# Kernel tuning notes

Hardware: AMD Instinct MI355X
Metric: run time of the kernel (lower is better)

## Reference

```python
import jax, jax.numpy as jnp
import numpy as np

COV_EMB = 32
N_HEAD = 2
FACTOR_TCL = 2   # TemporalConvolutionalLayer factor (default 2)
FACTOR_MLP = 1   # MLP factor passed from MultiAttention init
EPS = 1e-5


def _conv1d_causal(x, w, b):
    # x: [N, C, T], w: [O, C, 3]; torch pads 2 both sides then slices [..., :-2],
    # equivalent to left-pad 2 only -> output length T.
    y = jax.lax.conv_general_dilated(x, w, window_strides=(1,), padding=[(2, 0)],
                                     dimension_numbers=('NCH', 'OIH', 'NCH'))
    return y + b[None, :, None]


def _tcl(x, w_conv, b_conv, w_proj, b_proj):
    # TemporalConvolutionalLayer: x [..., T, C] -> [..., T, C]
    shp = x.shape
    T, C = shp[-2], shp[-1]
    x2 = x.reshape(-1, T, C).transpose(0, 2, 1)              # [N, C, T]
    h = jax.nn.gelu(_conv1d_causal(x2, w_conv, b_conv), approximate=False)
    h = h.transpose(0, 2, 1)                                  # [N, T, 2C]
    out = h @ w_proj.T + b_proj                               # [N, T, C]
    return out.reshape(*shp[:-1], C)


def _layernorm(x, w):
    mu = jnp.mean(x, axis=-1, keepdims=True)
    var = jnp.var(x, axis=-1, keepdims=True)
    return (x - mu) * jax.lax.rsqrt(var + EPS) * w


def setup_inputs() -> dict:
    key = jax.random.key(0)
    ks = jax.random.split(key, 20)
    C = COV_EMB
    C2 = FACTOR_TCL * C
    s = 0.02
    inp = {
        'causal_decoder': jax.random.normal(ks[0], (8, 4, 1024, C), jnp.float32),
        'past_kv': jax.random.normal(ks[1], (8, 1024, C), jnp.float32),
    }
    def tcl_params(i):
        return (jax.random.normal(ks[i], (C2, C, 3), jnp.float32) * s,
                jnp.zeros((C2,), jnp.float32),
                jax.random.normal(ks[i + 1], (C, C2), jnp.float32) * s,
                jnp.zeros((C,), jnp.float32))
    inp['wq_conv'], inp['bq_conv'], inp['wq_proj'], inp['bq_proj'] = tcl_params(2)
    inp['wk_conv'], inp['bk_conv'], inp['wk_proj'], inp['bk_proj'] = tcl_params(4)
    inp['wv_conv'], inp['bv_conv'], inp['wv_proj'], inp['bv_proj'] = tcl_params(6)
    inp['w_cproj'] = jax.random.normal(ks[8], (C, C), jnp.float32) * s   # bias=False
    inp['ln_w'] = jnp.ones((C,), jnp.float32)                            # bias=False
    inp['w_fc'] = jax.random.normal(ks[9], (FACTOR_MLP * C, C), jnp.float32) * s   # bias=False
    inp['w_mlp_proj'] = jax.random.normal(ks[10], (C, FACTOR_MLP * C), jnp.float32) * s
    return inp


def reference(causal_decoder, past_kv,
              wq_conv, bq_conv, wq_proj, bq_proj,
              wk_conv, bk_conv, wk_proj, bk_proj,
              wv_conv, bv_conv, wv_proj, bv_proj,
              w_cproj, ln_w, w_fc, w_mlp_proj):
    B, F, T, C = causal_decoder.shape
    nh, hd = N_HEAD, C // N_HEAD

    q = _tcl(causal_decoder, wq_conv, bq_conv, wq_proj, bq_proj)   # [B,F,T,C]
    k = _tcl(past_kv, wk_conv, bk_conv, wk_proj, bk_proj)          # [B,S,C]
    v = _tcl(past_kv, wv_conv, bv_conv, wv_proj, bv_proj)          # [B,S,C]

    S = k.shape[1]
    q = q.reshape(B, F, T, nh, hd).transpose(0, 1, 3, 2, 4)        # [B,F,h,T,d]
    k = k.reshape(B, S, nh, hd).transpose(0, 2, 1, 3)              # [B,h,S,d]
    v = v.reshape(B, S, nh, hd).transpose(0, 2, 1, 3)              # [B,h,S,d]

    scale = 1.0 / jnp.sqrt(jnp.asarray(hd, q.dtype))
    scores = jnp.einsum('bfhtd,bhsd->bfhts', q, k) * scale          # [B,F,h,T,S]
    attn = jax.nn.softmax(scores, axis=-1)
    y = jnp.einsum('bfhts,bhsd->bfhtd', attn, v)                    # [B,F,h,T,d]
    y = y.transpose(0, 1, 3, 2, 4).reshape(B, F, T, C)

    out = causal_decoder + y @ w_cproj.T                            # resid_dropout = id (p=0)
    h = _layernorm(out, ln_w)
    mlp = jax.nn.gelu(h @ w_fc.T, approximate=False) @ w_mlp_proj.T
    out = out + mlp
    return out
```

## Files before the change

kernel.cpp:

```cpp
#include <hip/hip_runtime.h>
#include <hip/hip_bf16.h>

#define T_LEN 1024

typedef __attribute__((ext_vector_type(8))) short short8;
typedef __attribute__((ext_vector_type(4))) short short4v;
typedef __attribute__((ext_vector_type(4))) float float4v;
typedef __attribute__((ext_vector_type(2))) unsigned uint2v;
typedef __attribute__((ext_vector_type(4))) unsigned uint4v;

__device__ __forceinline__ float gelu_exact(float x) {
    return 0.5f * x * (1.0f + erff(x * 0.70710678118654752440f));
}
__device__ __forceinline__ unsigned short f2bf(float f) {
    unsigned u = __float_as_uint(f);
    u += 0x7fffu + ((u >> 16) & 1u);
    return (unsigned short)(u >> 16);
}
__device__ __forceinline__ unsigned pk2bf(float a, float b) {
    __hip_bfloat162 h = __float22bfloat162_rn(make_float2(a, b));
    unsigned u;
    __builtin_memcpy(&u, &h, 4);
    return u;
}
__device__ __forceinline__ float fexp2(float x) {
    float r;
    asm("v_exp_f32 %0, %1" : "=v"(r) : "v"(x));
    return r;
}

__device__ __forceinline__ short8 xpose_p(float4v t0, float4v t1) {
    unsigned u0 = pk2bf(t0.x, t0.y);
    unsigned u1 = pk2bf(t0.z, t0.w);
    unsigned u2 = pk2bf(t1.x, t1.y);
    unsigned u3 = pk2bf(t1.z, t1.w);
    uint2v r0 = __builtin_amdgcn_permlane32_swap(u0, u2, false, false);
    uint2v r1 = __builtin_amdgcn_permlane32_swap(u1, u3, false, false);
    uint2v r2 = __builtin_amdgcn_permlane16_swap(r0.x, r0.y, false, false);
    uint2v r3 = __builtin_amdgcn_permlane16_swap(r1.x, r1.y, false, false);
    uint4v p = { r2.x, r3.x, r2.y, r3.y };
    short8 f;
    __builtin_memcpy(&f, &p, 16);
    return f;
}

__global__ __launch_bounds__(256) void kv_tcl(
    const float* __restrict__ pkv,
    const float* __restrict__ wkc, const float* __restrict__ bkc,
    const float* __restrict__ wkp, const float* __restrict__ bkp,
    const float* __restrict__ wvc, const float* __restrict__ bvc,
    const float* __restrict__ wvp, const float* __restrict__ bvp,
    unsigned short* __restrict__ kbf, unsigned short* __restrict__ vtbf)
{
    __shared__ __align__(16) unsigned short Abuf[32 * 96];
    __shared__ __align__(16) unsigned short WbT[64 * 96];
    __shared__ __align__(16) unsigned short Hb[32 * 72];
    __shared__ __align__(16) unsigned short WpB[32 * 72];

    const int tid = threadIdx.x;
    const int gb = blockIdx.x;

    const float *wc, *bc, *wp, *bp;
    unsigned short* outb;
    int n, mode;
    if (gb < 256) { n = gb >> 5;         wc = wkc; bc = bkc; wp = wkp; bp = bkp; outb = kbf;  mode = 0; }
    else          { n = (gb - 256) >> 5; wc = wvc; bc = bvc; wp = wvp; bp = bvp; outb = vtbf; mode = 1; }
    const int t0 = (gb & 31) * 32;

#pragma unroll
    for (int it = 0; it < 3; ++it) {
        int s = (tid + it * 256) >> 3;
        int sub = tid & 7;
        int t = s / 3, tap = s - t * 3;
        int tau = t0 + t - 2 + tap;
        float4 xv = make_float4(0.f, 0.f, 0.f, 0.f);
        if (tau >= 0) xv = *(const float4*)&pkv[((size_t)n * T_LEN + tau) * 32 + sub * 4];
        short4v pk = { (short)f2bf(xv.x), (short)f2bf(xv.y),
                       (short)f2bf(xv.z), (short)f2bf(xv.w) };
        *(short4v*)&Abuf[t * 96 + tap * 32 + sub * 4] = pk;
    }
#pragma unroll
    for (int it = 0; it < 6; ++it) {
        int i4 = tid + it * 256;
        int idx = i4 * 4;
        int o = idx / 96, r = idx - o * 96;
        float4 w4 = *(const float4*)&wc[idx];
        float we[4] = { w4.x, w4.y, w4.z, w4.w };
#pragma unroll
        for (int e = 0; e < 4; ++e) {
            int re = r + e, c = re / 3, tap = re - c * 3;
            WbT[o * 96 + tap * 32 + c] = f2bf(we[e]);
        }
    }
#pragma unroll
    for (int it = 0; it < 2; ++it) {
        int i4 = tid + it * 256;
        int idx = i4 * 4;
        int c = idx >> 6, o = idx & 63;
        float4 w4 = *(const float4*)&wp[idx];
        short4v pk = { (short)f2bf(w4.x), (short)f2bf(w4.y),
                       (short)f2bf(w4.z), (short)f2bf(w4.w) };
        *(short4v*)&WpB[c * 72 + o] = pk;
    }

    const int w = tid >> 6;
    const int ln = tid & 63;
    const int sn = ln & 15;
    const int quad = ln >> 4;

    const float bcv = bc[w * 16 + sn];
    const int tmw = w & 1, cnw = w >> 1;
    const float bpv = bp[cnw * 16 + sn];

    __syncthreads();

    short8 b0 = *(const short8*)&WbT[(w * 16 + sn) * 96 + 0  + quad * 8];
    short8 b1 = *(const short8*)&WbT[(w * 16 + sn) * 96 + 32 + quad * 8];
    short8 b2 = *(const short8*)&WbT[(w * 16 + sn) * 96 + 64 + quad * 8];
    float4v zero = { 0.f, 0.f, 0.f, 0.f };
    float4v acc[2] = { zero, zero };
#pragma unroll
    for (int tm = 0; tm < 2; ++tm) {
        const unsigned short* ar = &Abuf[(tm * 16 + sn) * 96 + quad * 8];
        short8 a0 = *(const short8*)(ar + 0);
        short8 a1 = *(const short8*)(ar + 32);
        short8 a2 = *(const short8*)(ar + 64);
        acc[tm] = __builtin_amdgcn_mfma_f32_16x16x32_bf16(a0, b0, acc[tm], 0, 0, 0);
        acc[tm] = __builtin_amdgcn_mfma_f32_16x16x32_bf16(a1, b1, acc[tm], 0, 0, 0);
        acc[tm] = __builtin_amdgcn_mfma_f32_16x16x32_bf16(a2, b2, acc[tm], 0, 0, 0);
    }
#pragma unroll
    for (int tm = 0; tm < 2; ++tm) {
        float ge[4];
        ge[0] = gelu_exact(acc[tm].x + bcv);
        ge[1] = gelu_exact(acc[tm].y + bcv);
        ge[2] = gelu_exact(acc[tm].z + bcv);
        ge[3] = gelu_exact(acc[tm].w + bcv);
#pragma unroll
        for (int i = 0; i < 4; ++i)
            Hb[(tm * 16 + quad * 4 + i) * 72 + w * 16 + sn] = f2bf(ge[i]);
    }

    __syncthreads();

    const unsigned short* hr = &Hb[(tmw * 16 + sn) * 72 + quad * 8];
    short8 pa0 = *(const short8*)(hr + 0);
    short8 pa1 = *(const short8*)(hr + 32);
    short8 pb0 = *(const short8*)&WpB[(cnw * 16 + sn) * 72 + quad * 8];
    short8 pb1 = *(const short8*)&WpB[(cnw * 16 + sn) * 72 + 32 + quad * 8];
    float4v pacc = zero;
    pacc = __builtin_amdgcn_mfma_f32_16x16x32_bf16(pa0, pb0, pacc, 0, 0, 0);
    pacc = __builtin_amdgcn_mfma_f32_16x16x32_bf16(pa1, pb1, pacc, 0, 0, 0);

    float v[4] = { pacc.x + bpv, pacc.y + bpv, pacc.z + bpv, pacc.w + bpv };
#pragma unroll
    for (int i = 0; i < 4; ++i) {
        int t = tmw * 16 + quad * 4 + i;
        int c = cnw * 16 + sn;
        if (mode == 0) {
            outb[((size_t)n * T_LEN + t0 + t) * 32 + c] = f2bf(v[i]);
        } else {
            outb[((size_t)(n * 2 + cnw) * 16 + sn) * T_LEN + t0 + t] = f2bf(v[i]);
        }
    }
}

__global__ __launch_bounds__(1024, 8) void fused_qae(
    const float* __restrict__ cd,
    const float* __restrict__ wqc, const float* __restrict__ bqc,
    const float* __restrict__ wqp, const float* __restrict__ bqp,
    const unsigned short* __restrict__ kbf,
    const unsigned short* __restrict__ vtbf,
    const float* __restrict__ wcp, const float* __restrict__ lnw,
    const float* __restrict__ wfc, const float* __restrict__ wmp,
    float* __restrict__ out)
{
    __shared__ __align__(16) char smem[52736];
    unsigned short* Abuf = (unsigned short*)(smem);
    unsigned short* WbT  = (unsigned short*)(smem + 12288);
    unsigned short* Hb   = (unsigned short*)(smem + 24576);
    unsigned short* WpB  = (unsigned short*)(smem + 33792);
    unsigned short* qs   = (unsigned short*)(smem + 38400);

    const int tid = threadIdx.x;
    const int bf = blockIdx.x >> 4;
    const int tt = blockIdx.x & 15;
    const int t0 = tt * 64;
    const int b = bf >> 2;
    const float SC = 0.36067376022224085f;

#pragma unroll
    for (int it = 0; it < 2; ++it) {
        int idx = tid + it * 1024;
        if (idx < 1536) {
            int s = idx >> 3;
            int sub = idx & 7;
            int t = s / 3, tap = s - t * 3;
            int tau = t0 + t - 2 + tap;
            float4 xv = make_float4(0.f, 0.f, 0.f, 0.f);
            if (tau >= 0) xv = *(const float4*)&cd[((size_t)bf * T_LEN + tau) * 32 + sub * 4];
            short4v pk = { (short)f2bf(xv.x), (short)f2bf(xv.y),
                           (short)f2bf(xv.z), (short)f2bf(xv.w) };
            *(short4v*)&Abuf[t * 96 + tap * 32 + sub * 4] = pk;
        }
    }
#pragma unroll
    for (int it = 0; it < 2; ++it) {
        int i4 = tid + it * 1024;
        if (i4 < 1536) {
            int idx = i4 * 4;
            int o = idx / 96, r = idx - o * 96;
            float4 w4 = *(const float4*)&wqc[idx];
            float we[4] = { w4.x, w4.y, w4.z, w4.w };
#pragma unroll
            for (int e = 0; e < 4; ++e) {
                int re = r + e, c = re / 3, tap = re - c * 3;
                WbT[o * 96 + tap * 32 + c] = f2bf(we[e]);
            }
        }
    }
    if (tid < 512) {
        int idx = tid * 4;
        int c = idx >> 6, o = idx & 63;
        float4 w4 = *(const float4*)&wqp[idx];
        short4v pk = { (short)f2bf(w4.x), (short)f2bf(w4.y),
                       (short)f2bf(w4.z), (short)f2bf(w4.w) };
        *(short4v*)&WpB[c * 72 + o] = pk;
    }

    const int w = tid >> 6;
    const int ln = tid & 63;
    const int sn = ln & 15;
    const int quad = ln >> 4;
    const float4v zero = { 0.f, 0.f, 0.f, 0.f };

    __syncthreads();

    {
        const int tm = w & 3;
        const int on = w >> 2;
        const unsigned short* ar = &Abuf[(tm * 16 + sn) * 96 + quad * 8];
        short8 a0 = *(const short8*)(ar + 0);
        short8 a1 = *(const short8*)(ar + 32);
        short8 a2 = *(const short8*)(ar + 64);
        const unsigned short* br = &WbT[(on * 16 + sn) * 96 + quad * 8];
        float4v c0 = zero;
        c0 = __builtin_amdgcn_mfma_f32_16x16x32_bf16(a0, *(const short8*)(br + 0),  c0, 0, 0, 0);
        c0 = __builtin_amdgcn_mfma_f32_16x16x32_bf16(a1, *(const short8*)(br + 32), c0, 0, 0, 0);
        c0 = __builtin_amdgcn_mfma_f32_16x16x32_bf16(a2, *(const short8*)(br + 64), c0, 0, 0, 0);
        const float bc0 = bqc[on * 16 + sn];
        float g0[4] = { gelu_exact(c0.x + bc0), gelu_exact(c0.y + bc0),
                        gelu_exact(c0.z + bc0), gelu_exact(c0.w + bc0) };
#pragma unroll
        for (int i = 0; i < 4; ++i)
            Hb[(tm * 16 + quad * 4 + i) * 72 + on * 16 + sn] = f2bf(g0[i]);
    }
    __syncthreads();

    if (w < 8) {
        const int tm = w & 3, cn = w >> 2;
        const unsigned short* hr = &Hb[(tm * 16 + sn) * 72 + quad * 8];
        short8 pa0 = *(const short8*)(hr + 0);
        short8 pa1 = *(const short8*)(hr + 32);
        const unsigned short* wr_ = &WpB[(cn * 16 + sn) * 72 + quad * 8];
        short8 pb0 = *(const short8*)(wr_ + 0);
        short8 pb1 = *(const short8*)(wr_ + 32);
        float4v pacc = zero;
        pacc = __builtin_amdgcn_mfma_f32_16x16x32_bf16(pa0, pb0, pacc, 0, 0, 0);
        pacc = __builtin_amdgcn_mfma_f32_16x16x32_bf16(pa1, pb1, pacc, 0, 0, 0);
        const float bpv = bqp[cn * 16 + sn];
        float v[4] = { (pacc.x + bpv) * SC, (pacc.y + bpv) * SC,
                       (pacc.z + bpv) * SC, (pacc.w + bpv) * SC };
#pragma unroll
        for (int i = 0; i < 4; ++i)
            qs[(tm * 16 + quad * 4 + i) * 40 + cn * 16 + sn] = f2bf(v[i]);
    } else {
        float* swc = (float*)(smem + 0);
        float* swf = (float*)(smem + 4608);
        float* swm = (float*)(smem + 9216);
        float* sln = (float*)(smem + 13824);
        int t2 = tid - 512;
        for (int i = t2; i < 1024; i += 512) {
            int r = i >> 5, cc = i & 31;
            swc[r * 36 + cc] = wcp[i];
            swf[r * 36 + cc] = wfc[i];
            swm[r * 36 + cc] = wmp[i];
        }
        if (t2 < 32) sln[t2] = lnw[t2];
    }
    __syncthreads();

    const int h = w & 1, rt = (w >> 1) & 3, sh = w >> 3;
    short8 aq = {0, 0, 0, 0, 0, 0, 0, 0};
    if (quad < 2)
        aq = *(const short8*)&qs[(rt * 16 + sn) * 40 + h * 16 + quad * 8];

    const unsigned short* kb = kbf + (size_t)b * T_LEN * 32 + h * 16 + quad * 8;
    const unsigned short* vb = vtbf + ((size_t)(b * 2 + h) * 16 + sn) * T_LEN + quad * 8;

    const short8 ones = { 16256, 16256, 16256, 16256,
                          16256, 16256, 16256, 16256 };
    float4v yacc = zero;
    float4v lacc = zero;

    int s0 = sh << 9;
#pragma unroll 2
    for (int ii = 0; ii < 8; ++ii, s0 += 64) {
        short8 ka0 = {0,0,0,0,0,0,0,0}, ka1 = ka0, kc0 = ka0, kc1 = ka0;
        if (quad < 2) {
            ka0 = *(const short8*)(kb + (size_t)(s0 + sn) * 32);
            ka1 = *(const short8*)(kb + (size_t)(s0 + 16 + sn) * 32);
            kc0 = *(const short8*)(kb + (size_t)(s0 + 32 + sn) * 32);
            kc1 = *(const short8*)(kb + (size_t)(s0 + 48 + sn) * 32);
        }
        short8 bvA = *(const short8*)(vb + s0);
        short8 bvB = *(const short8*)(vb + s0 + 32);

        float4v cA0 = __builtin_amdgcn_mfma_f32_16x16x32_bf16(ka0, aq, zero, 0, 0, 0);
        float4v cA1 = __builtin_amdgcn_mfma_f32_16x16x32_bf16(ka1, aq, zero, 0, 0, 0);
        float4v cB0 = __builtin_amdgcn_mfma_f32_16x16x32_bf16(kc0, aq, zero, 0, 0, 0);
        float4v cB1 = __builtin_amdgcn_mfma_f32_16x16x32_bf16(kc1, aq, zero, 0, 0, 0);

        float4v eA0, eA1, eB0, eB1;
        eA0.x = fexp2(cA0.x); eA0.y = fexp2(cA0.y); eA0.z = fexp2(cA0.z); eA0.w = fexp2(cA0.w);
        eA1.x = fexp2(cA1.x); eA1.y = fexp2(cA1.y); eA1.z = fexp2(cA1.z); eA1.w = fexp2(cA1.w);
        eB0.x = fexp2(cB0.x); eB0.y = fexp2(cB0.y); eB0.z = fexp2(cB0.z); eB0.w = fexp2(cB0.w);
        eB1.x = fexp2(cB1.x); eB1.y = fexp2(cB1.y); eB1.z = fexp2(cB1.z); eB1.w = fexp2(cB1.w);

        short8 apA = xpose_p(eA0, eA1);
        short8 apB = xpose_p(eB0, eB1);

        yacc = __builtin_amdgcn_mfma_f32_16x16x32_bf16(bvA, apA, yacc, 0, 0, 0);
        yacc = __builtin_amdgcn_mfma_f32_16x16x32_bf16(bvB, apB, yacc, 0, 0, 0);
        lacc = __builtin_amdgcn_mfma_f32_16x16x32_bf16(ones, apA, lacc, 0, 0, 0);
        lacc = __builtin_amdgcn_mfma_f32_16x16x32_bf16(ones, apB, lacc, 0, 0, 0);
    }

    {
        float* syp = (float*)(smem + (sh ? 43520 : 24576));
        *(float4v*)&syp[(rt * 16 + sn) * 32 + h * 16 + quad * 4] = yacc;
        float* lbuf = (float*)(smem + 51712);
        if (quad == 0) lbuf[(sh * 2 + h) * 64 + rt * 16 + sn] = lacc.x;
    }
    __syncthreads();

    float* swc = (float*)(smem + 0);
    float* swf = (float*)(smem + 4608);
    float* swm = (float*)(smem + 9216);
    float* sln = (float*)(smem + 13824);
    float* shn = (float*)(smem + 13952);
    float* sgv = (float*)(smem + 18560);
    float* sy0 = (float*)(smem + 24576);
    float* sy1 = (float*)(smem + 43520);
    float* lbuf = (float*)(smem + 51712);

    const int rl = tid >> 5, c = tid & 31;
    const float lnwc = sln[c];
#pragma unroll 1
    for (int p = 0; p < 2; ++p) {
        int r = p * 32 + rl;
        size_t row = (size_t)bf * T_LEN + t0 + r;
        const float li0 = 1.0f / (lbuf[r] + lbuf[128 + r]);
        const float li1 = 1.0f / (lbuf[64 + r] + lbuf[192 + r]);
        float x1 = cd[row * 32 + c];
#pragma unroll
        for (int j4 = 0; j4 < 8; ++j4) {
            const float sc = (j4 < 4) ? li0 : li1;
            int yi = r * 32 + j4 * 4;
            float4 y0 = *(const float4*)&sy0[yi];
            float4 y1 = *(const float4*)&sy1[yi];
            float4 yv = make_float4((y0.x + y1.x) * sc, (y0.y + y1.y) * sc,
                                    (y0.z + y1.z) * sc, (y0.w + y1.w) * sc);
            const float* wv = &swc[c * 36 + j4 * 4];
            x1 += wv[0] * yv.x + wv[1] * yv.y + wv[2] * yv.z + wv[3] * yv.w;
        }
        float s1 = x1, s2 = x1 * x1;
#pragma unroll
        for (int off = 16; off; off >>= 1) {
            s1 += __shfl_xor(s1, off);
            s2 += __shfl_xor(s2, off);
        }
        float mu = s1 * (1.0f / 32.0f);
        float var = s2 * (1.0f / 32.0f) - mu * mu;
        float hn = (x1 - mu) * rsqrtf(var + 1e-5f) * lnwc;
        shn[rl * 36 + c] = hn;
        float ga = 0.f;
#pragma unroll
        for (int j4 = 0; j4 < 8; ++j4) {
            float4 hv = *(const float4*)&shn[rl * 36 + j4 * 4];
            const float* wv = &swf[c * 36 + j4 * 4];
            ga += wv[0] * hv.x + wv[1] * hv.y + wv[2] * hv.z + wv[3] * hv.w;
        }
        float gv = gelu_exact(ga);
        sgv[rl * 36 + c] = gv;
        float oa = x1;
#pragma unroll
        for (int j4 = 0; j4 < 8; ++j4) {
            float4 gvv = *(const float4*)&sgv[rl * 36 + j4 * 4];
            const float* wv = &swm[c * 36 + j4 * 4];
            oa += wv[0] * gvv.x + wv[1] * gvv.y + wv[2] * gvv.z + wv[3] * gvv.w;
        }
        out[row * 32 + c] = oa;
    }
}

extern "C" void kernel_launch(void* const* d_in, const int* in_sizes, int n_in,
                              void* d_out, int out_size, void* d_ws, size_t ws_size,
                              hipStream_t stream) {
    const float* cd  = (const float*)d_in[0];
    const float* pkv = (const float*)d_in[1];
    const float* wqc = (const float*)d_in[2];
    const float* bqc = (const float*)d_in[3];
    const float* wqp = (const float*)d_in[4];
    const float* bqp = (const float*)d_in[5];
    const float* wkc = (const float*)d_in[6];
    const float* bkc = (const float*)d_in[7];
    const float* wkp = (const float*)d_in[8];
    const float* bkp = (const float*)d_in[9];
    const float* wvc = (const float*)d_in[10];
    const float* bvc = (const float*)d_in[11];
    const float* wvp = (const float*)d_in[12];
    const float* bvp = (const float*)d_in[13];
    const float* wcp = (const float*)d_in[14];
    const float* lnw = (const float*)d_in[15];
    const float* wfc = (const float*)d_in[16];
    const float* wmp = (const float*)d_in[17];

    unsigned short* kbf  = (unsigned short*)d_ws;
    unsigned short* vtbf = kbf + (size_t)8 * 1024 * 32;

    kv_tcl<<<512, 256, 0, stream>>>(pkv, wkc, bkc, wkp, bkp,
                                    wvc, bvc, wvp, bvp, kbf, vtbf);
    fused_qae<<<512, 1024, 0, stream>>>(cd, wqc, bqc, wqp, bqp, kbf, vtbf,
                                        wcp, lnw, wfc, wmp, (float*)d_out);
}
```

Before: 135.4 us.

## Fuse K/V TCL and query-attention kernels into one persistent mega-kernel with grid barrier

After: 207.1 us. 1.53x slower.

```diff
diff --git a/kernel.cpp b/kernel.cpp
--- a/kernel.cpp
+++ b/kernel.cpp
@@ -8,6 +8,8 @@
 typedef __attribute__((ext_vector_type(4))) float float4v;
 typedef __attribute__((ext_vector_type(2))) unsigned uint2v;
 typedef __attribute__((ext_vector_type(4))) unsigned uint4v;
+
+__device__ unsigned g_bar[2];
 
 __device__ __forceinline__ float gelu_exact(float x) {
     return 0.5f * x * (1.0f + erff(x * 0.70710678118654752440f));
@@ -44,189 +46,38 @@
     return f;
 }
 
-__global__ __launch_bounds__(256) void kv_tcl(
-    const float* __restrict__ pkv,
+__global__ __launch_bounds__(1024, 8) void mega(
+    const float* __restrict__ cd, const float* __restrict__ pkv,
+    const float* __restrict__ wqc, const float* __restrict__ bqc,
+    const float* __restrict__ wqp, const float* __restrict__ bqp,
     const float* __restrict__ wkc, const float* __restrict__ bkc,
     const float* __restrict__ wkp, const float* __restrict__ bkp,
     const float* __restrict__ wvc, const float* __restrict__ bvc,
     const float* __restrict__ wvp, const float* __restrict__ bvp,
-    unsigned short* __restrict__ kbf, unsigned short* __restrict__ vtbf)
-{
-    __shared__ __align__(16) unsigned short Abuf[32 * 96];
-    __shared__ __align__(16) unsigned short WbT[64 * 96];
-    __shared__ __align__(16) unsigned short Hb[32 * 72];
-    __shared__ __align__(16) unsigned short WpB[32 * 72];
-
-    const int tid = threadIdx.x;
-    const int gb = blockIdx.x;
-
-    const float *wc, *bc, *wp, *bp;
-    unsigned short* outb;
-    int n, mode;
-    if (gb < 256) { n = gb >> 5;         wc = wkc; bc = bkc; wp = wkp; bp = bkp; outb = kbf;  mode = 0; }
-    else          { n = (gb - 256) >> 5; wc = wvc; bc = bvc; wp = wvp; bp = bvp; outb = vtbf; mode = 1; }
-    const int t0 = (gb & 31) * 32;
-
-#pragma unroll
-    for (int it = 0; it < 3; ++it) {
-        int s = (tid + it * 256) >> 3;
-        int sub = tid & 7;
-        int t = s / 3, tap = s - t * 3;
-        int tau = t0 + t - 2 + tap;
-        float4 xv = make_float4(0.f, 0.f, 0.f, 0.f);
-        if (tau >= 0) xv = *(const float4*)&pkv[((size_t)n * T_LEN + tau) * 32 + sub * 4];
-        short4v pk = { (short)f2bf(xv.x), (short)f2bf(xv.y),
-                       (short)f2bf(xv.z), (short)f2bf(xv.w) };
-        *(short4v*)&Abuf[t * 96 + tap * 32 + sub * 4] = pk;
-    }
-#pragma unroll
-    for (int it = 0; it < 6; ++it) {
-        int i4 = tid + it * 256;
-        int idx = i4 * 4;
-        int o = idx / 96, r = idx - o * 96;
-        float4 w4 = *(const float4*)&wc[idx];
-        float we[4] = { w4.x, w4.y, w4.z, w4.w };
-#pragma unroll
-        for (int e = 0; e < 4; ++e) {
-            int re = r + e, c = re / 3, tap = re - c * 3;
-            WbT[o * 96 + tap * 32 + c] = f2bf(we[e]);
-        }
-    }
-#pragma unroll
-    for (int it = 0; it < 2; ++it) {
-        int i4 = tid + it * 256;
-        int idx = i4 * 4;
-        int c = idx >> 6, o = idx & 63;
-        float4 w4 = *(const float4*)&wp[idx];
-        short4v pk = { (short)f2bf(w4.x), (short)f2bf(w4.y),
-                       (short)f2bf(w4.z), (short)f2bf(w4.w) };
-        *(short4v*)&WpB[c * 72 + o] = pk;
-    }
-
-    const int w = tid >> 6;
-    const int ln = tid & 63;
-    const int sn = ln & 15;
-    const int quad = ln >> 4;
-
-    const float bcv = bc[w * 16 + sn];
-    const int tmw = w & 1, cnw = w >> 1;
-    const float bpv = bp[cnw * 16 + sn];
-
-    __syncthreads();
-
-    short8 b0 = *(const short8*)&WbT[(w * 16 + sn) * 96 + 0  + quad * 8];
-    short8 b1 = *(const short8*)&WbT[(w * 16 + sn) * 96 + 32 + quad * 8];
-    short8 b2 = *(const short8*)&WbT[(w * 16 + sn) * 96 + 64 + quad * 8];
-    float4v zero = { 0.f, 0.f, 0.f, 0.f };
-    float4v acc[2] = { zero, zero };
-#pragma unroll
-    for (int tm = 0; tm < 2; ++tm) {
-        const unsigned short* ar = &Abuf[(tm * 16 + sn) * 96 + quad * 8];
-        short8 a0 = *(const short8*)(ar + 0);
-        short8 a1 = *(const short8*)(ar + 32);
-        short8 a2 = *(const short8*)(ar + 64);
-        acc[tm] = __builtin_amdgcn_mfma_f32_16x16x32_bf16(a0, b0, acc[tm], 0, 0, 0);
-        acc[tm] = __builtin_amdgcn_mfma_f32_16x16x32_bf16(a1, b1, acc[tm], 0, 0, 0);
-        acc[tm] = __builtin_amdgcn_mfma_f32_16x16x32_bf16(a2, b2, acc[tm], 0, 0, 0);
-    }
-#pragma unroll
-    for (int tm = 0; tm < 2; ++tm) {
-        float ge[4];
-        ge[0] = gelu_exact(acc[tm].x + bcv);
-        ge[1] = gelu_exact(acc[tm].y + bcv);
-        ge[2] = gelu_exact(acc[tm].z + bcv);
-        ge[3] = gelu_exact(acc[tm].w + bcv);
-#pragma unroll
-        for (int i = 0; i < 4; ++i)
-            Hb[(tm * 16 + quad * 4 + i) * 72 + w * 16 + sn] = f2bf(ge[i]);
-    }
-
-    __syncthreads();
-
-    const unsigned short* hr = &Hb[(tmw * 16 + sn) * 72 + quad * 8];
-    short8 pa0 = *(const short8*)(hr + 0);
-    short8 pa1 = *(const short8*)(hr + 32);
-    short8 pb0 = *(const short8*)&WpB[(cnw * 16 + sn) * 72 + quad * 8];
-    short8 pb1 = *(const short8*)&WpB[(cnw * 16 + sn) * 72 + 32 + quad * 8];
-    float4v pacc = zero;
-    pacc = __builtin_amdgcn_mfma_f32_16x16x32_bf16(pa0, pb0, pacc, 0, 0, 0);
-    pacc = __builtin_amdgcn_mfma_f32_16x16x32_bf16(pa1, pb1, pacc, 0, 0, 0);
-
-    float v[4] = { pacc.x + bpv, pacc.y + bpv, pacc.z + bpv, pacc.w + bpv };
-#pragma unroll
-    for (int i = 0; i < 4; ++i) {
-        int t = tmw * 16 + quad * 4 + i;
-        int c = cnw * 16 + sn;
-        if (mode == 0) {
-            outb[((size_t)n * T_LEN + t0 + t) * 32 + c] = f2bf(v[i]);
-        } else {
-            outb[((size_t)(n * 2 + cnw) * 16 + sn) * T_LEN + t0 + t] = f2bf(v[i]);
-        }
-    }
-}
-
-__global__ __launch_bounds__(1024, 8) void fused_qae(
-    const float* __restrict__ cd,
-    const float* __restrict__ wqc, const float* __restrict__ bqc,
-    const float* __restrict__ wqp, const float* __restrict__ bqp,
-    const unsigned short* __restrict__ kbf,
-    const unsigned short* __restrict__ vtbf,
     const float* __restrict__ wcp, const float* __restrict__ lnw,
     const float* __restrict__ wfc, const float* __restrict__ wmp,
+    unsigned short* __restrict__ kbf, unsigned short* __restrict__ vtbf,
     float* __restrict__ out)
 {
-    __shared__ __align__(16) char smem[52736];
-    unsigned short* Abuf = (unsigned short*)(smem);
-    unsigned short* WbT  = (unsigned short*)(smem + 12288);
-    unsigned short* Hb   = (unsigned short*)(smem + 24576);
-    unsigned short* WpB  = (unsigned short*)(smem + 33792);
-    unsigned short* qs   = (unsigned short*)(smem + 38400);
+    __shared__ __align__(16) char smem[65536];
+    unsigned short* Abuf  = (unsigned short*)(smem);
+    unsigned short* WbT   = (unsigned short*)(smem + 12288);
+    unsigned short* Hb    = (unsigned short*)(smem + 24576);
+    unsigned short* WpB   = (unsigned short*)(smem + 33792);
+    unsigned short* WpBkv = (unsigned short*)(smem + 48640);
+    unsigned short* WbTkv = (unsigned short*)(smem + 53248);
 
     const int tid = threadIdx.x;
-    const int bf = blockIdx.x >> 4;
-    const int tt = blockIdx.x & 15;
-    const int t0 = tt * 64;
-    const int b = bf >> 2;
+    const int bid = blockIdx.x;
+    const int bf = bid >> 3;
+    const int b  = bid >> 5;
+    const int kvmode = bid >> 7;
+    const int kn = (bid >> 4) & 7;
+    const float* wc_kv = kvmode ? wvc : wkc;
+    const float* bc_kv = kvmode ? bvc : bkc;
+    const float* wp_kv = kvmode ? wvp : wkp;
+    const float* bp_kv = kvmode ? bvp : bkp;
     const float SC = 0.36067376022224085f;
-
-#pragma unroll
-    for (int it = 0; it < 2; ++it) {
-        int idx = tid + it * 1024;
-        if (idx < 1536) {
-            int s = idx >> 3;
-            int sub = idx & 7;
-            int t = s / 3, tap = s - t * 3;
-            int tau = t0 + t - 2 + tap;
-            float4 xv = make_float4(0.f, 0.f, 0.f, 0.f);
-            if (tau >= 0) xv = *(const float4*)&cd[((size_t)bf * T_LEN + tau) * 32 + sub * 4];
-            short4v pk = { (short)f2bf(xv.x), (short)f2bf(xv.y),
-                           (short)f2bf(xv.z), (short)f2bf(xv.w) };
-            *(short4v*)&Abuf[t * 96 + tap * 32 + sub * 4] = pk;
-        }
-    }
-#pragma unroll
-    for (int it = 0; it < 2; ++it) {
-        int i4 = tid + it * 1024;
-        if (i4 < 1536) {
-            int idx = i4 * 4;
-            int o = idx / 96, r = idx - o * 96;
-            float4 w4 = *(const float4*)&wqc[idx];
-            float we[4] = { w4.x, w4.y, w4.z, w4.w };
-#pragma unroll
-            for (int e = 0; e < 4; ++e) {
-                int re = r + e, c = re / 3, tap = re - c * 3;
-                WbT[o * 96 + tap * 32 + c] = f2bf(we[e]);
-            }
-        }
-    }
-    if (tid < 512) {
-        int idx = tid * 4;
-        int c = idx >> 6, o = idx & 63;
-        float4 w4 = *(const float4*)&wqp[idx];
-        short4v pk = { (short)f2bf(w4.x), (short)f2bf(w4.y),
-                       (short)f2bf(w4.z), (short)f2bf(w4.w) };
-        *(short4v*)&WpB[c * 72 + o] = pk;
-    }
 
     const int w = tid >> 6;
     const int ln = tid & 63;
@@ -234,173 +85,336 @@
     const int quad = ln >> 4;
     const float4v zero = { 0.f, 0.f, 0.f, 0.f };
 
-    __syncthreads();
-
-    {
-        const int tm = w & 3;
-        const int on = w >> 2;
-        const unsigned short* ar = &Abuf[(tm * 16 + sn) * 96 + quad * 8];
-        short8 a0 = *(const short8*)(ar + 0);
-        short8 a1 = *(const short8*)(ar + 32);
-        short8 a2 = *(const short8*)(ar + 64);
-        const unsigned short* br = &WbT[(on * 16 + sn) * 96 + quad * 8];
-        float4v c0 = zero;
-        c0 = __builtin_amdgcn_mfma_f32_16x16x32_bf16(a0, *(const short8*)(br + 0),  c0, 0, 0, 0);
-        c0 = __builtin_amdgcn_mfma_f32_16x16x32_bf16(a1, *(const short8*)(br + 32), c0, 0, 0, 0);
-        c0 = __builtin_amdgcn_mfma_f32_16x16x32_bf16(a2, *(const short8*)(br + 64), c0, 0, 0, 0);
-        const float bc0 = bqc[on * 16 + sn];
-        float g0[4] = { gelu_exact(c0.x + bc0), gelu_exact(c0.y + bc0),
-                        gelu_exact(c0.z + bc0), gelu_exact(c0.w + bc0) };
-#pragma unroll
-        for (int i = 0; i < 4; ++i)
-            Hb[(tm * 16 + quad * 4 + i) * 72 + on * 16 + sn] = f2bf(g0[i]);
+#pragma unroll 1
+    for (int pass = 0; pass < 2; ++pass) {
+        const int tile = (bid << 1) | pass;
+        const int t0  = (tile & 15) * 64;
+        const int kt0 = (tile & 31) * 32;
+        unsigned short* qs = (unsigned short*)(smem + 38400 + pass * 5120);
+
+#pragma unroll
+        for (int it = 0; it < 2; ++it) {
+            int idx = tid + it * 1024;
+            if (idx < 1536) {
+                int s = idx >> 3;
+                int sub = idx & 7;
+                int t = s / 3, tap = s - t * 3;
+                int tau = t0 + t - 2 + tap;
+                float4 xv = make_float4(0.f, 0.f, 0.f, 0.f);
+                if (tau >= 0) xv = *(const float4*)&cd[((size_t)bf * T_LEN + tau) * 32 + sub * 4];
+                short4v pk = { (short)f2bf(xv.x), (short)f2bf(xv.y),
+                               (short)f2bf(xv.z), (short)f2bf(xv.w) };
+                *(short4v*)&Abuf[t * 96 + tap * 32 + sub * 4] = pk;
+            }
+        }
+        if (pass == 0) {
+#pragma unroll
+            for (int it = 0; it < 2; ++it) {
+                int i4 = tid + it * 1024;
+                if (i4 < 1536) {
+                    int idx = i4 * 4;
+                    int o = idx / 96, r = idx - o * 96;
+                    float4 w4 = *(const float4*)&wqc[idx];
+                    float we[4] = { w4.x, w4.y, w4.z, w4.w };
+#pragma unroll
+                    for (int e = 0; e < 4; ++e) {
+                        int re = r + e, c = re / 3, tap = re - c * 3;
+                        WbT[o * 96 + tap * 32 + c] = f2bf(we[e]);
+                    }
+                }
+            }
+            if (tid < 512) {
+                int idx = tid * 4;
+                int c = idx >> 6, o = idx & 63;
+                float4 w4 = *(const float4*)&wqp[idx];
+                short4v pk = { (short)f2bf(w4.x), (short)f2bf(w4.y),
+                               (short)f2bf(w4.z), (short)f2bf(w4.w) };
+                *(short4v*)&WpB[c * 72 + o] = pk;
+            }
+        }
+        __syncthreads();
+
+        {
+            const int tm = w & 3;
+            const int on = w >> 2;
+            const unsigned short* ar = &Abuf[(tm * 16 + sn) * 96 + quad * 8];
+            short8 a0 = *(const short8*)(ar + 0);
+            short8 a1 = *(const short8*)(ar + 32);
+            short8 a2 = *(const short8*)(ar + 64);
+            const unsigned short* br = &WbT[(on * 16 + sn) * 96 + quad * 8];
+            float4v c0 = zero;
+            c0 = __builtin_amdgcn_mfma_f32_16x16x32_bf16(a0, *(const short8*)(br + 0),  c0, 0, 0, 0);
+            c0 = __builtin_amdgcn_mfma_f32_16x16x32_bf16(a1, *(const short8*)(br + 32), c0, 0, 0, 0);
+            c0 = __builtin_amdgcn_mfma_f32_16x16x32_bf16(a2, *(const short8*)(br + 64), c0, 0, 0, 0);
+            const float bc0 = bqc[on * 16 + sn];
+            float g0[4] = { gelu_exact(c0.x + bc0), gelu_exact(c0.y + bc0),
+                            gelu_exact(c0.z + bc0), gelu_exact(c0.w + bc0) };
+#pragma unroll
+            for (int i = 0; i < 4; ++i)
+                Hb[(tm * 16 + quad * 4 + i) * 72 + on * 16 + sn] = f2bf(g0[i]);
+        }
+        __syncthreads();
+
+        if (w < 8) {
+            const int tm = w & 3, cn = w >> 2;
+            const unsigned short* hr = &Hb[(tm * 16 + sn) * 72 + quad * 8];
+            short8 pa0 = *(const short8*)(hr + 0);
+            short8 pa1 = *(const short8*)(hr + 32);
+            const unsigned short* wr_ = &WpB[(cn * 16 + sn) * 72 + quad * 8];
+            short8 pb0 = *(const short8*)(wr_ + 0);
+            short8 pb1 = *(const short8*)(wr_ + 32);
+            float4v pacc = zero;
+            pacc = __builtin_amdgcn_mfma_f32_16x16x32_bf16(pa0, pb0, pacc, 0, 0, 0);
+            pacc = __builtin_amdgcn_mfma_f32_16x16x32_bf16(pa1, pb1, pacc, 0, 0, 0);
+            const float bpv = bqp[cn * 16 + sn];
+            float v[4] = { (pacc.x + bpv) * SC, (pacc.y + bpv) * SC,
+                           (pacc.z + bpv) * SC, (pacc.w + bpv) * SC };
+#pragma unroll
+            for (int i = 0; i < 4; ++i)
+                qs[(tm * 16 + quad * 4 + i) * 40 + cn * 16 + sn] = f2bf(v[i]);
+        } else {
+            const int t2 = tid - 512;
+#pragma unroll
+            for (int it = 0; it < 2; ++it) {
+                int idx = t2 + it * 512;
+                if (idx < 768) {
+                    int s = idx >> 3;
+                    int sub = idx & 7;
+                    int t = s / 3, tap = s - t * 3;
+                    int tau = kt0 + t - 2 + tap;
+                    float4 xv = make_float4(0.f, 0.f, 0.f, 0.f);
+                    if (tau >= 0) xv = *(const float4*)&pkv[((size_t)kn * T_LEN + tau) * 32 + sub * 4];
+                    short4v pk = { (short)f2bf(xv.x), (short)f2bf(xv.y),
+                                   (short)f2bf(xv.z), (short)f2bf(xv.w) };
+                    *(short4v*)&Abuf[t * 96 + tap * 32 + sub * 4] = pk;
+                }
+            }
+            if (pass == 0) {
+#pragma unroll
+                for (int it = 0; it < 3; ++it) {
+                    int i4 = t2 + it * 512;
+                    int idx = i4 * 4;
+                    int o = idx / 96, r = idx - o * 96;
+                    float4 w4 = *(const float4*)&wc_kv[idx];
+                    float we[4] = { w4.x, w4.y, w4.z, w4.w };
+#pragma unroll
+                    for (int e = 0; e < 4; ++e) {
+                        int re = r + e, c = re / 3, tap = re - c * 3;
+                        WbTkv[o * 96 + tap * 32 + c] = f2bf(we[e]);
+                    }
+                }
+                {
+                    int idx = t2 * 4;
+                    int c = idx >> 6, o = idx & 63;
+                    float4 w4 = *(const float4*)&wp_kv[idx];
+                    short4v pk = { (short)f2bf(w4.x), (short)f2bf(w4.y),
+                                   (short)f2bf(w4.z), (short)f2bf(w4.w) };
+                    *(short4v*)&WpBkv[c * 72 + o] = pk;
+                }
+            }
+        }
+        __syncthreads();
+
+        if (w < 8) {
+            const int tm = w & 1;
+            const int on = w >> 1;
+            const unsigned short* ar = &Abuf[(tm * 16 + sn) * 96 + quad * 8];
+            short8 a0 = *(const short8*)(ar + 0);
+            short8 a1 = *(const short8*)(ar + 32);
+            short8 a2 = *(const short8*)(ar + 64);
+            const unsigned short* br = &WbTkv[(on * 16 + sn) * 96 + quad * 8];
+            float4v c0 = zero;
+            c0 = __builtin_amdgcn_mfma_f32_16x16x32_bf16(a0, *(const short8*)(br + 0),  c0, 0, 0, 0);
+            c0 = __builtin_amdgcn_mfma_f32_16x16x32_bf16(a1, *(const short8*)(br + 32), c0, 0, 0, 0);
+            c0 = __builtin_amdgcn_mfma_f32_16x16x32_bf16(a2, *(const short8*)(br + 64), c0, 0, 0, 0);
+            const float bc0 = bc_kv[on * 16 + sn];
+            float g0[4] = { gelu_exact(c0.x + bc0), gelu_exact(c0.y + bc0),
+                            gelu_exact(c0.z + bc0), gelu_exact(c0.w + bc0) };
+#pragma unroll
+            for (int i = 0; i < 4; ++i)
+                Hb[(tm * 16 + quad * 4 + i) * 72 + on * 16 + sn] = f2bf(g0[i]);
+        }
+        __syncthreads();
+
+        if (w < 4) {
+            const int tm = w & 1, cn = w >> 1;
+            const unsigned short* hr = &Hb[(tm * 16 + sn) * 72 + quad * 8];
+            short8 pa0 = *(const short8*)(hr + 0);
+            short8 pa1 = *(const short8*)(hr + 32);
+            const unsigned short* wr_ = &WpBkv[(cn * 16 + sn) * 72 + quad * 8];
+            short8 pb0 = *(const short8*)(wr_ + 0);
+            short8 pb1 = *(const short8*)(wr_ + 32);
+            float4v pacc = zero;
+            pacc = __builtin_amdgcn_mfma_f32_16x16x32_bf16(pa0, pb0, pacc, 0, 0, 0);
+            pacc = __builtin_amdgcn_mfma_f32_16x16x32_bf16(pa1, pb1, pacc, 0, 0, 0);
+            const float bpv = bp_kv[cn * 16 + sn];
+            float vv[4] = { pacc.x + bpv, pacc.y + bpv, pacc.z + bpv, pacc.w + bpv };
+#pragma unroll
+            for (int i = 0; i < 4; ++i) {
+                int t = tm * 16 + quad * 4 + i;
+                int c = cn * 16 + sn;
+                if (kvmode == 0) {
+                    kbf[((size_t)kn * T_LEN + kt0 + t) * 32 + c] = f2bf(vv[i]);
+                } else {
+                    vtbf[((size_t)(kn * 2 + cn) * 16 + sn) * T_LEN + kt0 + t] = f2bf(vv[i]);
+                }
+            }
+        }
+        __syncthreads();
+    }
+
+    if (tid == 0) {
+        __threadfence();
+        __hip_atomic_fetch_add(&g_bar[0], 1u, __ATOMIC_SEQ_CST, __HIP_MEMORY_SCOPE_AGENT);
+        unsigned sp = 0;
+        while (__hip_atomic_load(&g_bar[0], __ATOMIC_SEQ_CST, __HIP_MEMORY_SCOPE_AGENT) < 256u) {
+            if (++sp > (1u << 20)) break;
+            __builtin_amdgcn_s_sleep(2);
+        }
+        __threadfence();
+        unsigned o2 = __hip_atomic_fetch_add(&g_bar[1], 1u, __ATOMIC_SEQ_CST, __HIP_MEMORY_SCOPE_AGENT);
+        if (o2 == 255u) {
+            __hip_atomic_store(&g_bar[0], 0u, __ATOMIC_SEQ_CST, __HIP_MEMORY_SCOPE_AGENT);
+            __hip_atomic_store(&g_bar[1], 0u, __ATOMIC_SEQ_CST, __HIP_MEMORY_SCOPE_AGENT);
+        }
     }
     __syncthreads();
 
-    if (w < 8) {
-        const int tm = w & 3, cn = w >> 2;
-        const unsigned short* hr = &Hb[(tm * 16 + sn) * 72 + quad * 8];
-        short8 pa0 = *(const short8*)(hr + 0);
-        short8 pa1 = *(const short8*)(hr + 32);
-        const unsigned short* wr_ = &WpB[(cn * 16 + sn) * 72 + quad * 8];
-        short8 pb0 = *(const short8*)(wr_ + 0);
-        short8 pb1 = *(const short8*)(wr_ + 32);
-        float4v pacc = zero;
-        pacc = __builtin_amdgcn_mfma_f32_16x16x32_bf16(pa0, pb0, pacc, 0, 0, 0);
-        pacc = __builtin_amdgcn_mfma_f32_16x16x32_bf16(pa1, pb1, pacc, 0, 0, 0);
-        const float bpv = bqp[cn * 16 + sn];
-        float v[4] = { (pacc.x + bpv) * SC, (pacc.y + bpv) * SC,
-                       (pacc.z + bpv) * SC, (pacc.w + bpv) * SC };
-#pragma unroll
-        for (int i = 0; i < 4; ++i)
-            qs[(tm * 16 + quad * 4 + i) * 40 + cn * 16 + sn] = f2bf(v[i]);
-    } else {
+    {
         float* swc = (float*)(smem + 0);
         float* swf = (float*)(smem + 4608);
         float* swm = (float*)(smem + 9216);
         float* sln = (float*)(smem + 13824);
-        int t2 = tid - 512;
-        for (int i = t2; i < 1024; i += 512) {
-            int r = i >> 5, cc = i & 31;
-            swc[r * 36 + cc] = wcp[i];
-            swf[r * 36 + cc] = wfc[i];
-            swm[r * 36 + cc] = wmp[i];
-        }
-        if (t2 < 32) sln[t2] = lnw[t2];
+        int r = tid >> 5, cc = tid & 31;
+        swc[r * 36 + cc] = wcp[tid];
+        swf[r * 36 + cc] = wfc[tid];
+        swm[r * 36 + cc] = wmp[tid];
+        if (tid < 32) sln[tid] = lnw[tid];
     }
     __syncthreads();
 
-    const int h = w & 1, rt = (w >> 1) & 3, sh = w >> 3;
-    short8 aq = {0, 0, 0, 0, 0, 0, 0, 0};
-    if (quad < 2)
-        aq = *(const short8*)&qs[(rt * 16 + sn) * 40 + h * 16 + quad * 8];
-
-    const unsigned short* kb = kbf + (size_t)b * T_LEN * 32 + h * 16 + quad * 8;
-    const unsigned short* vb = vtbf + ((size_t)(b * 2 + h) * 16 + sn) * T_LEN + quad * 8;
-
     const short8 ones = { 16256, 16256, 16256, 16256,
                           16256, 16256, 16256, 16256 };
-    float4v yacc = zero;
-    float4v lacc = zero;
-
-    int s0 = sh << 9;
+    const unsigned short* kb_base = kbf + (size_t)b * T_LEN * 32;
+    const unsigned short* vb_base = vtbf + (size_t)b * 2 * 16 * T_LEN;
+
+#pragma unroll 1
+    for (int pass = 0; pass < 2; ++pass) {
+        const int tile = (bid << 1) | pass;
+        const int t0 = (tile & 15) * 64;
+        unsigned short* qs = (unsigned short*)(smem + 38400 + pass * 5120);
+        if (pass) __syncthreads();
+
+        const int h = w & 1, rt = (w >> 1) & 3, sh = w >> 3;
+        short8 aq = {0, 0, 0, 0, 0, 0, 0, 0};
+        if (quad < 2)
+            aq = *(const short8*)&qs[(rt * 16 + sn) * 40 + h * 16 + quad * 8];
+
+        const unsigned short* kb = kb_base + h * 16 + quad * 8;
+        const unsigned short* vb = vb_base + ((size_t)h * 16 + sn) * T_LEN + quad * 8;
+
+        float4v yacc = zero;
+        float4v lacc = zero;
+
+        int s0 = sh << 9;
 #pragma unroll 2
-    for (int ii = 0; ii < 8; ++ii, s0 += 64) {
-        short8 ka0 = {0,0,0,0,0,0,0,0}, ka1 = ka0, kc0 = ka0, kc1 = ka0;
-        if (quad < 2) {
-            ka0 = *(const short8*)(kb + (size_t)(s0 + sn) * 32);
-            ka1 = *(const short8*)(kb + (size_t)(s0 + 16 + sn) * 32);
-            kc0 = *(const short8*)(kb + (size_t)(s0 + 32 + sn) * 32);
-            kc1 = *(const short8*)(kb + (size_t)(s0 + 48 + sn) * 32);
-        }
-        short8 bvA = *(const short8*)(vb + s0);
-        short8 bvB = *(const short8*)(vb + s0 + 32);
-
-        float4v cA0 = __builtin_amdgcn_mfma_f32_16x16x32_bf16(ka0, aq, zero, 0, 0, 0);
-        float4v cA1 = __builtin_amdgcn_mfma_f32_16x16x32_bf16(ka1, aq, zero, 0, 0, 0);
-        float4v cB0 = __builtin_amdgcn_mfma_f32_16x16x32_bf16(kc0, aq, zero, 0, 0, 0);
-        float4v cB1 = __builtin_amdgcn_mfma_f32_16x16x32_bf16(kc1, aq, zero, 0, 0, 0);
-
-        float4v eA0, eA1, eB0, eB1;
-        eA0.x = fexp2(cA0.x); eA0.y = fexp2(cA0.y); eA0.z = fexp2(cA0.z); eA0.w = fexp2(cA0.w);
-        eA1.x = fexp2(cA1.x); eA1.y = fexp2(cA1.y); eA1.z = fexp2(cA1.z); eA1.w = fexp2(cA1.w);
-        eB0.x = fexp2(cB0.x); eB0.y = fexp2(cB0.y); eB0.z = fexp2(cB0.z); eB0.w = fexp2(cB0.w);
-        eB1.x = fexp2(cB1.x); eB1.y = fexp2(cB1.y); eB1.z = fexp2(cB1.z); eB1.w = fexp2(cB1.w);
-
-        short8 apA = xpose_p(eA0, eA1);
-        short8 apB = xpose_p(eB0, eB1);
-
-        yacc = __builtin_amdgcn_mfma_f32_16x16x32_bf16(bvA, apA, yacc, 0, 0, 0);
-        yacc = __builtin_amdgcn_mfma_f32_16x16x32_bf16(bvB, apB, yacc, 0, 0, 0);
-        lacc = __builtin_amdgcn_mfma_f32_16x16x32_bf16(ones, apA, lacc, 0, 0, 0);
-        lacc = __builtin_amdgcn_mfma_f32_16x16x32_bf16(ones, apB, lacc, 0, 0, 0);
-    }
-
-    {
-        float* syp = (float*)(smem + (sh ? 43520 : 24576));
-        *(float4v*)&syp[(rt * 16 + sn) * 32 + h * 16 + quad * 4] = yacc;
-        float* lbuf = (float*)(smem + 51712);
-        if (quad == 0) lbuf[(sh * 2 + h) * 64 + rt * 16 + sn] = lacc.x;
-    }
-    __syncthreads();
-
-    float* swc = (float*)(smem + 0);
-    float* swf = (float*)(smem + 4608);
-    float* swm = (float*)(smem + 9216);
-    float* sln = (float*)(smem + 13824);
-    float* shn = (float*)(smem + 13952);
-    float* sgv = (float*)(smem + 18560);
-    float* sy0 = (float*)(smem + 24576);
-    float* sy1 = (float*)(smem + 43520);
-    float* lbuf = (float*)(smem + 51712);
-
-    const int rl = tid >> 5, c = tid & 31;
-    const float lnwc = sln[c];
+        for (int ii = 0; ii < 8; ++ii, s0 += 64) {
+            short8 ka0 = {0,0,0,0,0,0,0,0}, ka1 = ka0, kc0 = ka0, kc1 = ka0;
+            if (quad < 2) {
+                ka0 = *(const short8*)(kb + (size_t)(s0 + sn) * 32);
+                ka1 = *(const short8*)(kb + (size_t)(s0 + 16 + sn) * 32);
+                kc0 = *(const short8*)(kb + (size_t)(s0 + 32 + sn) * 32);
+                kc1 = *(const short8*)(kb + (size_t)(s0 + 48 + sn) * 32);
+            }
+            short8 bvA = *(const short8*)(vb + s0);
+            short8 bvB = *(const short8*)(vb + s0 + 32);
+
+            float4v cA0 = __builtin_amdgcn_mfma_f32_16x16x32_bf16(ka0, aq, zero, 0, 0, 0);
+            float4v cA1 = __builtin_amdgcn_mfma_f32_16x16x32_bf16(ka1, aq, zero, 0, 0, 0);
+            float4v cB0 = __builtin_amdgcn_mfma_f32_16x16x32_bf16(kc0, aq, zero, 0, 0, 0);
+            float4v cB1 = __builtin_amdgcn_mfma_f32_16x16x32_bf16(kc1, aq, zero, 0, 0, 0);
+
+            float4v eA0, eA1, eB0, eB1;
+            eA0.x = fexp2(cA0.x); eA0.y = fexp2(cA0.y); eA0.z = fexp2(cA0.z); eA0.w = fexp2(cA0.w);
+            eA1.x = fexp2(cA1.x); eA1.y = fexp2(cA1.y); eA1.z = fexp2(cA1.z); eA1.w = fexp2(cA1.w);
+            eB0.x = fexp2(cB0.x); eB0.y = fexp2(cB0.y); eB0.z = fexp2(cB0.z); eB0.w = fexp2(cB0.w);
+            eB1.x = fexp2(cB1.x); eB1.y = fexp2(cB1.y); eB1.z = fexp2(cB1.z); eB1.w = fexp2(cB1.w);
+
+            short8 apA = xpose_p(eA0, eA1);
+            short8 apB = xpose_p(eB0, eB1);
+
+            yacc = __builtin_amdgcn_mfma_f32_16x16x32_bf16(bvA, apA, yacc, 0, 0, 0);
+            yacc = __builtin_amdgcn_mfma_f32_16x16x32_bf16(bvB, apB, yacc, 0, 0, 0);
+            lacc = __builtin_amdgcn_mfma_f32_16x16x32_bf16(ones, apA, lacc, 0, 0, 0);
+            lacc = __builtin_amdgcn_mfma_f32_16x16x32_bf16(ones, apB, lacc, 0, 0, 0);
+        }
+
+        {
+            float* syp = (float*)(smem + (sh ? 48640 : 24576));
+            *(float4v*)&syp[(rt * 16 + sn) * 32 + h * 16 + quad * 4] = yacc;
+            float* lbuf = (float*)(smem + 32768);
+            if (quad == 0) lbuf[(sh * 2 + h) * 64 + rt * 16 + sn] = lacc.x;
+        }
+        __syncthreads();
+
+        float* swc = (float*)(smem + 0);
+        float* swf = (float*)(smem + 4608);
+        float* swm = (float*)(smem + 9216);
+        float* sln = (float*)(smem + 13824);
+        float* shn = (float*)(smem + 13952);
+        float* sgv = (float*)(smem + 18560);
+        float* sy0 = (float*)(smem + 24576);
+        float* sy1 = (float*)(smem + 48640);
+        float* lbuf = (float*)(smem + 32768);
+
+        const int rl = tid >> 5, c = tid & 31;
+        const float lnwc = sln[c];
 #pragma unroll 1
-    for (int p = 0; p < 2; ++p) {
-        int r = p * 32 + rl;
-        size_t row = (size_t)bf * T_LEN + t0 + r;
-        const float li0 = 1.0f / (lbuf[r] + lbuf[128 + r]);
-        const float li1 = 1.0f / (lbuf[64 + r] + lbuf[192 + r]);
-        float x1 = cd[row * 32 + c];
-#pragma unroll
-        for (int j4 = 0; j4 < 8; ++j4) {
-            const float sc = (j4 < 4) ? li0 : li1;
-            int yi = r * 32 + j4 * 4;
-            float4 y0 = *(const float4*)&sy0[yi];
-            float4 y1 = *(const float4*)&sy1[yi];
-            float4 yv = make_float4((y0.x + y1.x) * sc, (y0.y + y1.y) * sc,
-                                    (y0.z + y1.z) * sc, (y0.w + y1.w) * sc);
-            const float* wv = &swc[c * 36 + j4 * 4];
-            x1 += wv[0] * yv.x + wv[1] * yv.y + wv[2] * yv.z + wv[3] * yv.w;
-        }
-        float s1 = x1, s2 = x1 * x1;
-#pragma unroll
-        for (int off = 16; off; off >>= 1) {
-            s1 += __shfl_xor(s1, off);
-            s2 += __shfl_xor(s2, off);
-        }
-        float mu = s1 * (1.0f / 32.0f);
-        float var = s2 * (1.0f / 32.0f) - mu * mu;
-        float hn = (x1 - mu) * rsqrtf(var + 1e-5f) * lnwc;
-        shn[rl * 36 + c] = hn;
-        float ga = 0.f;
-#pragma unroll
-        for (int j4 = 0; j4 < 8; ++j4) {
-            float4 hv = *(const float4*)&shn[rl * 36 + j4 * 4];
-            const float* wv = &swf[c * 36 + j4 * 4];
-            ga += wv[0] * hv.x + wv[1] * hv.y + wv[2] * hv.z + wv[3] * hv.w;
-        }
-        float gv = gelu_exact(ga);
-        sgv[rl * 36 + c] = gv;
-        float oa = x1;
-#pragma unroll
-        for (int j4 = 0; j4 < 8; ++j4) {
-            float4 gvv = *(const float4*)&sgv[rl * 36 + j4 * 4];
-            const float* wv = &swm[c * 36 + j4 * 4];
-            oa += wv[0] * gvv.x + wv[1] * gvv.y + wv[2] * gvv.z + wv[3] * gvv.w;
-        }
-        out[row * 32 + c] = oa;
+        for (int p = 0; p < 2; ++p) {
+            int r = p * 32 + rl;
+            size_t row = (size_t)bf * T_LEN + t0 + r;
+            const float li0 = 1.0f / (lbuf[r] + lbuf[128 + r]);
+            const float li1 = 1.0f / (lbuf[64 + r] + lbuf[192 + r]);
+            float x1 = cd[row * 32 + c];
+#pragma unroll
+            for (int j4 = 0; j4 < 8; ++j4) {
+                const float sc = (j4 < 4) ? li0 : li1;
+                int yi = r * 32 + j4 * 4;
+                float4 y0 = *(const float4*)&sy0[yi];
+                float4 y1 = *(const float4*)&sy1[yi];
+                float4 yv = make_float4((y0.x + y1.x) * sc, (y0.y + y1.y) * sc,
+                                        (y0.z + y1.z) * sc, (y0.w + y1.w) * sc);
+                const float* wv = &swc[c * 36 + j4 * 4];
+                x1 += wv[0] * yv.x + wv[1] * yv.y + wv[2] * yv.z + wv[3] * yv.w;
+            }
+            float s1 = x1, s2 = x1 * x1;
+#pragma unroll
+            for (int off = 16; off; off >>= 1) {
+                s1 += __shfl_xor(s1, off);
+                s2 += __shfl_xor(s2, off);
+            }
+            float mu = s1 * (1.0f / 32.0f);
+            float var = s2 * (1.0f / 32.0f) - mu * mu;
+            float hn = (x1 - mu) * rsqrtf(var + 1e-5f) * lnwc;
+            shn[rl * 36 + c] = hn;
+            float ga = 0.f;
+#pragma unroll
+            for (int j4 = 0; j4 < 8; ++j4) {
+                float4 hv = *(const float4*)&shn[rl * 36 + j4 * 4];
+                const float* wv = &swf[c * 36 + j4 * 4];
+                ga += wv[0] * hv.x + wv[1] * hv.y + wv[2] * hv.z + wv[3] * hv.w;
+            }
+            float gv = gelu_exact(ga);
+            sgv[rl * 36 + c] = gv;
+            float oa = x1;
+#pragma unroll
+            for (int j4 = 0; j4 < 8; ++j4) {
+                float4 gvv = *(const float4*)&sgv[rl * 36 + j4 * 4];
+                const float* wv = &swm[c * 36 + j4 * 4];
+                oa += wv[0] * gvv.x + wv[1] * gvv.y + wv[2] * gvv.z + wv[3] * gvv.w;
+            }
+            out[row * 32 + c] = oa;
+        }
     }
 }
 
@@ -429,8 +443,7 @@
     unsigned short* kbf  = (unsigned short*)d_ws;
     unsigned short* vtbf = kbf + (size_t)8 * 1024 * 32;
 
-    kv_tcl<<<512, 256, 0, stream>>>(pkv, wkc, bkc, wkp, bkp,
-                                    wvc, bvc, wvp, bvp, kbf, vtbf);
-    fused_qae<<<512, 1024, 0, stream>>>(cd, wqc, bqc, wqp, bqp, kbf, vtbf,
-                                        wcp, lnw, wfc, wmp, (float*)d_out);
-}
+    mega<<<256, 1024, 0, stream>>>(cd, pkv, wqc, bqc, wqp, bqp,
+                                   wkc, bkc, wkp, bkp, wvc, bvc, wvp, bvp,
+                                   wcp, lnw, wfc, wmp, kbf, vtbf, (float*)d_out);
+}
```
